# Optimization experiments

Measured on AMD Instinct MI355X. Metric: run time of the kernel, lower is better.

Reference implementation:

```python
import jax, jax.numpy as jnp
import numpy as np

N_ROOMS = 126          # len(building.rooms)
N = 2 + N_ROOMS        # state dim (reset_iv: 2 + n_rooms)
M = 1 + N_ROOMS        # input dim u = [Tout, Q_watts...]
T = 200000             # number of eval times
DT = 30.0              # seconds between eval points
TOUT_DT = 3600.0       # outside-temp table grid spacing (s)
K = 1700               # table length (covers 1000 + T*DT seconds)
LOAD_MAX = 500.0       # physical_loads_scaling: W/m^2 upper bound


def setup_inputs() -> dict:
    key = jax.random.key(0)
    ks = jax.random.split(key, 6)
    # Stable RC-style state matrix: negative diagonal dominates
    A = 1e-5 * jax.random.normal(ks[0], (N, N), dtype=jnp.float32) - 2e-4 * jnp.eye(N, dtype=jnp.float32)
    B = 1e-6 * jax.random.normal(ks[1], (N, M), dtype=jnp.float32)
    loads = jax.random.normal(ks[2], (2, N_ROOMS), dtype=jnp.float32)   # raw params (pre-sigmoid)
    areas = 10.0 + 40.0 * jax.random.uniform(ks[3], (N_ROOMS,), dtype=jnp.float32)  # room areas m^2
    Tout_vals = 10.0 + 5.0 * jax.random.normal(ks[4], (K,), dtype=jnp.float32)      # hourly Tout table
    t_eval = 1000.0 + DT * jnp.arange(T, dtype=jnp.float32)
    iv = 26.0 * jnp.ones((N, 1), dtype=jnp.float32)
    return {"A": A, "B": B, "loads": loads, "areas": areas,
            "Tout_vals": Tout_vals, "t_eval": t_eval, "iv": iv, "action": 1}


def _interp_tout(vals, t):
    # linear interpolation on a uniform grid starting at t=0 (replaces scipy interp1d)
    pos = t / TOUT_DT
    idx = jnp.clip(jnp.floor(pos).astype(jnp.int32), 0, K - 2)
    w = pos - idx.astype(pos.dtype)
    return vals[idx] * (1.0 - w) + vals[idx + 1] * w


def reference(A, B, loads, areas, Tout_vals, t_eval, iv, action):
    t0 = t_eval[0]
    ts = t_eval - t0
    # _build_loads: sigmoid transform + physical scaling
    lp = jax.nn.sigmoid(loads) * LOAD_MAX
    cool_load, gain_load = lp[0], lp[1]
    # f_ode constants: Q_area = -cool*action + gain; Q_watts = proportional_heating
    Q_watts = (-cool_load * action + gain_load) * areas        # [n_rooms]
    b_q = B[:, 1:] @ Q_watts                                   # [N] constant forcing
    b_T = B[:, 0]                                              # [N] Tout coupling
    x0 = iv[:, 0]

    def f(t, x):
        Tout = _interp_tout(Tout_vals, t + t0)
        return A @ x + b_T * Tout + b_q

    # torchdiffeq method='rk4' -> rk4_alt_step_func (3/8 rule)
    def step(x, tt):
        t, tn = tt
        dt = tn - t
        k1 = f(t, x)
        k2 = f(t + dt / 3.0, x + dt * k1 / 3.0)
        k3 = f(t + dt * 2.0 / 3.0, x + dt * (k2 - k1 / 3.0))
        k4 = f(t + dt, x + dt * (k1 - k2 + k3))
        xn = x + dt * (k1 + 3.0 * (k2 + k3) + k4) / 8.0
        return xn, xn

    _, traj = jax.lax.scan(step, x0, (ts[:-1], ts[1:]))
    out = jnp.concatenate([x0[None, :], traj], axis=0)         # [T, N]
    return out[..., None]                                      # [T, N, 1] matching iv shape
```

## Files before the change

### kernel.cpp

```cpp
#include <hip/hip_runtime.h>

#define N 128
#define NR 126
#define MBCOL 127
#define TSTEPS 200000
#define L1 49
#define C1 4096
#define KT 1700

#define OFF_Z     0
#define OFF_S     16384
#define OFF_P     32768
#define OFF_PW2   65536
#define OFF_PW4   81920
#define OFF_PW8   98304
#define OFF_PW16  114688
#define OFF_PW32  131072
#define OFF_Q     147456
#define OFF_WC    180224
#define OFF_ACC   212992
#define OFF_DELTA 737280
#define OFF_B1    753664
#define OFF_B2    1015808
#define OFF_B3    1146880
#define OFF_A16   1212416
#define OFF_C1    1245184
#define OFF_C2    1261568
#define OFF_C3    1269760
#define OFF_BST16 753664
#define OFF_Q256  786432

typedef float v4f __attribute__((ext_vector_type(4)));
typedef __attribute__((ext_vector_type(8))) short bf16x8;
typedef __attribute__((ext_vector_type(4))) float f32x4;

#define OFF_PEH   65536
#define OFF_PEL   75776

#define LBAR() do { \
  __builtin_amdgcn_sched_barrier(0); \
  asm volatile("s_waitcnt lgkmcnt(0)" ::: "memory"); \
  __builtin_amdgcn_sched_barrier(0); \
  __builtin_amdgcn_s_barrier(); \
  __builtin_amdgcn_sched_barrier(0); \
} while (0)

#define GLD4(dst, p) \
  asm volatile("global_load_dwordx4 %0, %1, off" : "=v"(dst) : "v"(p))
#define PINQ(q) \
  asm volatile("s_waitcnt vmcnt(0)" \
    : "+v"(q[0]),"+v"(q[1]),"+v"(q[2]),"+v"(q[3]), \
      "+v"(q[4]),"+v"(q[5]),"+v"(q[6]),"+v"(q[7]), \
      "+v"(q[8]),"+v"(q[9]),"+v"(q[10]),"+v"(q[11]), \
      "+v"(q[12]),"+v"(q[13]),"+v"(q[14]),"+v"(q[15]))
#define PINQ8(q) \
  asm volatile("s_waitcnt vmcnt(0)" \
    : "+v"(q[0]),"+v"(q[1]),"+v"(q[2]),"+v"(q[3]), \
      "+v"(q[4]),"+v"(q[5]),"+v"(q[6]),"+v"(q[7]))

__device__ __forceinline__ void loadQ16(v4f* qv, const float* pb)
{
  #pragma unroll
  for (int s = 0; s < 16; ++s) GLD4(qv[s], pb + 4*s);
  PINQ(qv);
}

__device__ __forceinline__ void bsplit(float f, unsigned short& h, unsigned short& l)
{
  unsigned int u = __float_as_uint(f);
  unsigned int r = (u + 0x7FFFu + ((u >> 16) & 1u)) >> 16;
  float hf = __uint_as_float(r << 16);
  h = (unsigned short)r;
  float lo = f - hf;
  unsigned int u2 = __float_as_uint(lo);
  unsigned int r2 = (u2 + 0x7FFFu + ((u2 >> 16) & 1u)) >> 16;
  l = (unsigned short)r2;
}

__device__ __forceinline__ void mmRowS(const float* __restrict__ Aw,
                                       const float* __restrict__ Bw,
                                       float* __restrict__ Cw,
                                       float* __restrict__ Cw2,
                                       float* __restrict__ sm, int r, float scale)
{
  int t = threadIdx.x, c = t & 127, kh = t >> 7;
  const float* Ar = Aw + r*N + kh*64;
  const float* Bc = Bw + (kh*64)*N + c;
  float p0=0.f, p1=0.f, p2=0.f, p3=0.f;
  #pragma unroll 4
  for (int s = 0; s < 64; s += 4) {
    const float4 av = *(const float4*)(Ar + s);
    p0 = fmaf(av.x, Bc[(s+0)*N], p0);
    p1 = fmaf(av.y, Bc[(s+1)*N], p1);
    p2 = fmaf(av.z, Bc[(s+2)*N], p2);
    p3 = fmaf(av.w, Bc[(s+3)*N], p3);
  }
  sm[kh*128 + c] = (p0+p1)+(p2+p3);
  __syncthreads();
  if (kh == 0) {
    float v = (sm[c] + sm[128 + c]) * scale;
    Cw[r*N + c] = v;
    if (Cw2) Cw2[r*N + c] = v;
  }
}

#define mmRowR(Aw,Bw,Cw,Cw2,sm,r) mmRowS(Aw,Bw,Cw,Cw2,sm,r,1.0f)

__device__ void prepLite(const float* __restrict__ A, const float* __restrict__ B,
                         const float* __restrict__ loads, const float* __restrict__ areas,
                         const float* __restrict__ iv, const int* __restrict__ action,
                         float* __restrict__ ws, float* __restrict__ out,
                         float* __restrict__ sm)
{
  float* qw = sm;
  float* ys = sm + 128;
  float* qs = sm + 640;
  int t = threadIdx.x;
  float actf = (float)action[0];
  if (t < NR) {
    float lc = (1.0f / (1.0f + expf(-loads[t]))) * 500.0f;
    float lg = (1.0f / (1.0f + expf(-loads[NR + t]))) * 500.0f;
    qw[t] = (-lc * actf + lg) * areas[t];
  }
  __syncthreads();
  if (t < N) {
    float bq = 0.0f;
    for (int i = 0; i < NR; ++i) bq += B[t * MBCOL + 1 + i] * qw[i];
    ys[t] = B[t * MBCOL];
    qs[t] = bq;
  }
  __syncthreads();
  for (int s = 1; s < 4; ++s) {
    if (t < N) {
      float ay = 0.0f, aq = 0.0f;
      for (int k = 0; k < N; ++k) {
        float a = A[t * N + k];
        ay += a * ys[(s-1)*N + k];
        aq += a * qs[(s-1)*N + k];
      }
      ys[s*N + t] = 30.0f * ay;
      qs[s*N + t] = 30.0f * aq;
    }
    __syncthreads();
  }
  if (t < N) {
    float y0 = ys[t], y1 = ys[N+t], y2 = ys[2*N+t], y3 = ys[3*N+t];
    float q0 = qs[t], q1 = qs[N+t], q2 = qs[2*N+t], q3 = qs[3*N+t];
    ws[OFF_WC + (0*L1)*N + t] = 3.75f * (y0 + y1 + y2*(1.0f/3.0f) + y3*(1.0f/3.0f));
    ws[OFF_WC + (1*L1)*N + t] = 3.75f * (3.0f*y0 + 2.0f*y1 + y2);
    ws[OFF_WC + (2*L1)*N + t] = 3.75f * (3.0f*y0 + y1);
    ws[OFF_WC + (3*L1)*N + t] = 3.75f * y0;
    ws[OFF_WC + (4*L1)*N + t] = 3.75f * (8.0f*q0 + 4.0f*q1 + (4.0f/3.0f)*q2 + (1.0f/3.0f)*q3);
    out[t] = iv[t];
  }
}

__device__ __forceinline__ void polyRowA(const float* __restrict__ A,
                                         float* __restrict__ ws,
                                         float* __restrict__ sm)
{
  int t = threadIdx.x, c = t & 127, kh = t >> 7;
  int r = blockIdx.x;
  const float* S = ws + OFF_S;
  const float* Sr = S + r*N + kh*64;
  float x3=0.f, x4=0.f;
  #pragma unroll 4
  for (int s = 0; s < 64; s += 4) {
    const float4 av = *(const float4*)(Sr + s);
    int k = kh*64 + s;
    x3 = fmaf(av.x, A[(k+0)*N+c], x3); x3 = fmaf(av.y, A[(k+1)*N+c], x3);
    x3 = fmaf(av.z, A[(k+2)*N+c], x3); x3 = fmaf(av.w, A[(k+3)*N+c], x3);
    x4 = fmaf(av.x, S[(k+0)*N+c], x4); x4 = fmaf(av.y, S[(k+1)*N+c], x4);
    x4 = fmaf(av.z, S[(k+2)*N+c], x4); x4 = fmaf(av.w, S[(k+3)*N+c], x4);
  }
  sm[kh*128 + c] = x3;
  sm[256 + kh*128 + c] = x4;
  __syncthreads();
  if (kh == 0) {
    float a3 = 30.0f * (sm[c] + sm[128+c]);
    float a4 = sm[256+c] + sm[384+c];
    float pv = (r==c ? 1.0f : 0.0f) + 30.0f*A[r*N+c] + 0.5f*S[r*N+c]
             + (1.0f/6.0f)*a3 + (1.0f/24.0f)*a4;
    ws[OFF_P + r*N + c] = pv;
  }
}

__device__ __forceinline__ void wUnit(const float* __restrict__ Pw,
                                      float* __restrict__ ws,
                                      int uw, int wbase, int wcount,
                                      float* __restrict__ wbuf )
{
  int t = threadIdx.x;
  int np = 5 * wcount;
  for (int i = t; i < 8*N; i += 256) {
    int pl = i >> 7, k = i & 127;
    int p = uw*8 + pl;
    float v = 0.0f;
    if (p < np) {
      int m = p / wcount, kk = p % wcount;
      v = ws[OFF_WC + (m*L1 + kk)*N + k];
    }
    wbuf[pl*N + k] = v;
  }
  __syncthreads();
  int r = t & 127, pg = t >> 7;
  float acc[4] = {0,0,0,0};
  #pragma unroll 2
  for (int k = 0; k < N; k += 4) {
    const float4 av = *(const float4*)(Pw + r*N + k);
    #pragma unroll
    for (int pi = 0; pi < 4; ++pi) {
      const float4 wv = *(const float4*)(wbuf + (pg*4+pi)*N + k);
      acc[pi] = fmaf(av.x, wv.x, acc[pi]);
      acc[pi] = fmaf(av.y, wv.y, acc[pi]);
      acc[pi] = fmaf(av.z, wv.z, acc[pi]);
      acc[pi] = fmaf(av.w, wv.w, acc[pi]);
    }
  }
  #pragma unroll
  for (int pi = 0; pi < 4; ++pi) {
    int p = uw*8 + pg*4 + pi;
    if (p < np) {
      int m = p / wcount, kk = p % wcount;
      ws[OFF_WC + (m*L1 + wbase + kk)*N + r] = acc[pi];
    }
  }
}

__device__ __forceinline__ void treeUnit(const float* __restrict__ Qm,
                                         const float* __restrict__ src,
                                         float* __restrict__ dst,
                                         int uw, float* __restrict__ wbuf)
{
  int t = threadIdx.x;
  for (int i = t; i < 8*N; i += 256) {
    int pl = i >> 7, k = i & 127;
    wbuf[pl*N + k] = src[(size_t)(2*(uw*8 + pl))*N + k];
  }
  __syncthreads();
  int r = t & 127, pg = t >> 7;
  float acc[4] = {0,0,0,0};
  #pragma unroll 2
  for (int k = 0; k < N; k += 4) {
    const float4 av = *(const float4*)(Qm + r*N + k);
    #pragma unroll
    for (int pi = 0; pi < 4; ++pi) {
      const float4 wv = *(const float4*)(wbuf + (pg*4+pi)*N + k);
      acc[pi] = fmaf(av.x, wv.x, acc[pi]);
      acc[pi] = fmaf(av.y, wv.y, acc[pi]);
      acc[pi] = fmaf(av.z, wv.z, acc[pi]);
      acc[pi] = fmaf(av.w, wv.w, acc[pi]);
    }
  }
  #pragma unroll
  for (int pi = 0; pi < 4; ++pi) {
    int j = uw*8 + pg*4 + pi;
    dst[(size_t)j*N + r] = acc[pi] + src[(size_t)(2*j + 1)*N + r];
  }
}

__global__ __launch_bounds__(256) void kPhase(
    const float* __restrict__ A, const float* __restrict__ B,
    const float* __restrict__ loads, const float* __restrict__ areas,
    const float* __restrict__ iv, const int* __restrict__ action,
    float* __restrict__ ws, float* __restrict__ out, int ph)
{
  __shared__ float sm[1280];
  int b = blockIdx.x;
  if (ph >= 20) {
    int lv = ph - 20;
    const int srcO[7] = {OFF_ACC, OFF_B1, OFF_B2, OFF_B3, OFF_A16, OFF_C1, OFF_C2};
    const int dstO[7] = {OFF_B1, OFF_B2, OFF_B3, OFF_A16, OFF_C1, OFF_C2, OFF_C3};
    const int nco[7]  = {2048, 1024, 512, 256, 128, 64, 32};
    const int qO[7]   = {OFF_Q, OFF_S, OFF_P, OFF_PW8, OFF_PW16, OFF_PW32, OFF_Z};
    const int pS[7]   = {OFF_S, OFF_P, OFF_PW8, OFF_PW16, OFF_PW32, OFF_Z, OFF_DELTA};
    const int pD[7]   = {OFF_P, OFF_PW8, OFF_PW16, OFF_PW32, OFF_Z, OFF_DELTA, OFF_Q256};
    int nb = nco[lv] >> 3;
    if (b < nb) treeUnit(ws + qO[lv], ws + srcO[lv], ws + dstO[lv], b, sm);
    else mmRowR(ws + pS[lv], ws + pS[lv], ws + pD[lv], nullptr, sm, b - nb);
    return;
  }
  if (ph == 1) {
    if (b < 128) mmRowS(A, A, ws+OFF_S, nullptr, sm, b, 900.0f);
    else prepLite(A, B, loads, areas, iv, action, ws, out, sm);
    return;
  }
  if (ph == 2) { polyRowA(A, ws, sm); return; }
  if (ph <= 8) {
    int s = ph - 3;
    const int srcOff[6] = {OFF_P, OFF_PW2, OFF_PW4, OFF_PW8, OFF_PW16, OFF_PW32};
    const int dstOff[6] = {OFF_PW2, OFF_PW4, OFF_PW8, OFF_PW16, OFF_PW32, OFF_S};
    if (b < 128) {
      if (s < 5) mmRowR(ws+srcOff[s], ws+srcOff[s], ws+dstOff[s], nullptr, sm, b);
      else       mmRowR(ws+OFF_PW32, ws+OFF_PW16, ws+OFF_S, nullptr, sm, b);
    } else {
      int wbase  = (s < 5) ? (1 << s) : 32;
      int wcount = (s < 5) ? (1 << s) : 17;
      wUnit(ws + srcOff[s], ws, b - 128, wbase, wcount, sm);
    }
    return;
  }
  if (ph == 9) {
    if (b < 128) {
      mmRowR(ws+OFF_S, ws+OFF_P, ws+OFF_Z, ws+OFF_Q, sm, b);
    } else {
      int r = b - 128;
      int tt = threadIdx.x;
      if (tt < 160) {
        float val;
        if (tt < 128)      val = ws[OFF_P + r*N + tt];
        else if (tt < 133) val = ws[OFF_WC + ((tt-128)*L1)*N + r];
        else               val = 0.0f;
        unsigned short h, l2;
        bsplit(val, h, l2);
        ((unsigned short*)(ws + OFF_PEH))[r*160 + tt] = h;
        ((unsigned short*)(ws + OFF_PEL))[r*160 + tt] = l2;
      }
    }
    return;
  }
}

__device__ __forceinline__ void build_table(float* lt, const float* __restrict__ Tout,
                                            int J0, int t, int cnt, int stride)
{
  int tbase = 1470*J0 + 1000;
  for (int s = t; s < cnt; s += stride) {
    float tt = (float)(tbase + 10*s);
    float pos = tt / 3600.0f;
    int idx = (int)pos;
    if (idx > KT-2) idx = KT-2;
    float w = pos - (float)idx;
    lt[s] = Tout[idx]*(1.0f-w) + Tout[idx+1]*w;
  }
}

__global__ __launch_bounds__(256) void k3_acc(const float* __restrict__ Tout,
                                              float* __restrict__ ws)
{
  __shared__ float lt[1184];
  int t = threadIdx.x;
  if (blockIdx.x >= 512) {
    mmRowR(ws+OFF_Z, ws+OFF_Z, ws+OFF_S, nullptr, lt, blockIdx.x - 512);
    return;
  }
  int J0 = blockIdx.x * 8;
  build_table(lt, Tout, J0, t, 1177, 256);
  __syncthreads();
  int r = t & 127, jh = t >> 7;
  float a[4] = {0.0f, 0.0f, 0.0f, 0.0f};
  for (int k = 0; k < L1; ++k) {
    float w0 = ws[OFF_WC + (0*L1+k)*N + r];
    float w1 = ws[OFF_WC + (1*L1+k)*N + r];
    float w2 = ws[OFF_WC + (2*L1+k)*N + r];
    float w3 = ws[OFF_WC + (3*L1+k)*N + r];
    float w4 = ws[OFF_WC + (4*L1+k)*N + r];
    #pragma unroll
    for (int q = 0; q < 4; ++q) {
      int cl = jh*4 + q;
      int soff = 3*(L1*cl + (L1-1) - k);
      a[q] += w0*lt[soff] + w1*lt[soff+1] + w2*lt[soff+2] + w3*lt[soff+3] + w4;
    }
  }
  #pragma unroll
  for (int q = 0; q < 4; ++q)
    ws[OFF_ACC + (size_t)(J0 + jh*4 + q)*N + r] = a[q];
}

__device__ __forceinline__ void mv_step3(const v4f* qv, float* x, float* ps,
                                         int r, int kh, float addv)
{
  const v4f* xp = (const v4f*)(x + kh*64);
  float p0=0.f, p1=0.f, p2=0.f, p3=0.f;
  #pragma unroll
  for (int s = 0; s < 16; s += 4) {
    v4f x0 = xp[s+0], x1 = xp[s+1], x2 = xp[s+2], x3 = xp[s+3];
    p0 = fmaf(qv[s+0][0],x0[0],p0); p0 = fmaf(qv[s+0][1],x0[1],p0);
    p0 = fmaf(qv[s+0][2],x0[2],p0); p0 = fmaf(qv[s+0][3],x0[3],p0);
    p1 = fmaf(qv[s+1][0],x1[0],p1); p1 = fmaf(qv[s+1][1],x1[1],p1);
    p1 = fmaf(qv[s+1][2],x1[2],p1); p1 = fmaf(qv[s+1][3],x1[3],p1);
    p2 = fmaf(qv[s+2][0],x2[0],p2); p2 = fmaf(qv[s+2][1],x2[1],p2);
    p2 = fmaf(qv[s+2][2],x2[2],p2); p2 = fmaf(qv[s+2][3],x2[3],p2);
    p3 = fmaf(qv[s+3][0],x3[0],p3); p3 = fmaf(qv[s+3][1],x3[1],p3);
    p3 = fmaf(qv[s+3][2],x3[2],p3); p3 = fmaf(qv[s+3][3],x3[3],p3);
  }
  ps[kh*128 + r] = (p0+p1)+(p2+p3);
  LBAR();
  if (kh == 0) x[r] = ps[r] + ps[128 + r] + addv;
  LBAR();
}

__global__ __launch_bounds__(256, 2) void k5ab(const float* __restrict__ iv,
                                               float* __restrict__ ws)
{
  __shared__ float x[N];
  __shared__ float ps[256];
  __shared__ float c3[32*N];
  __shared__ float aq[15*N];
  __shared__ float a16d[15*N];
  int t = threadIdx.x, r = t & 127, kh = t >> 7;
  int p = blockIdx.x;
  for (int i = t; i < 32*N; i += 256) c3[i] = ws[OFF_C3 + i];
  for (int i = t; i < 15*N; i += 256) a16d[i] = ws[OFF_A16 + (size_t)(p*16)*N + i];
  if (t < N) x[t] = iv[t];
  v4f qv[16];
  loadQ16(qv, ws + OFF_DELTA + r*N + kh*64);
  __syncthreads();
  for (int q = 0; q < p; ++q) {
    const v4f* xp = (const v4f*)(c3 + (size_t)(2*q)*N + kh*64);
    float p0=0.f, p1=0.f, p2=0.f, p3=0.f;
    #pragma unroll
    for (int s = 0; s < 16; s += 4) {
      v4f x0 = xp[s+0], x1 = xp[s+1], x2 = xp[s+2], x3 = xp[s+3];
      p0 = fmaf(qv[s+0][0],x0[0],p0); p0 = fmaf(qv[s+0][1],x0[1],p0);
      p0 = fmaf(qv[s+0][2],x0[2],p0); p0 = fmaf(qv[s+0][3],x0[3],p0);
      p1 = fmaf(qv[s+1][0],x1[0],p1); p1 = fmaf(qv[s+1][1],x1[1],p1);
      p1 = fmaf(qv[s+1][2],x1[2],p1); p1 = fmaf(qv[s+1][3],x1[3],p1);
      p2 = fmaf(qv[s+2][0],x2[0],p2); p2 = fmaf(qv[s+2][1],x2[1],p2);
      p2 = fmaf(qv[s+2][2],x2[2],p2); p2 = fmaf(qv[s+2][3],x2[3],p2);
      p3 = fmaf(qv[s+3][0],x3[0],p3); p3 = fmaf(qv[s+3][1],x3[1],p3);
      p3 = fmaf(qv[s+3][2],x3[2],p3); p3 = fmaf(qv[s+3][3],x3[3],p3);
    }
    ps[kh*128 + r] = (p0+p1)+(p2+p3);
    LBAR();
    if (kh == 0) aq[q*N + r] = ps[r] + ps[128 + r] + c3[(size_t)(2*q+1)*N + r];
    LBAR();
  }
  loadQ16(qv, ws + OFF_Q256 + r*N + kh*64);
  __syncthreads();
  for (int q = 0; q < p; ++q)
    mv_step3(qv, x, ps, r, kh, aq[q*N + r]);
  loadQ16(qv, ws + OFF_PW16 + r*N + kh*64);
  __syncthreads();
  for (int i = 0; i < 16; ++i) {
    if (kh == 0) ws[OFF_BST16 + (size_t)(p*16 + i)*N + r] = x[r];
    if (i == 15) break;
    mv_step3(qv, x, ps, r, kh, a16d[i*N + r]);
  }
}

__global__ __launch_bounds__(512) void k7_main(const float* __restrict__ Tout,
                                               const float* __restrict__ ws,
                                               float* __restrict__ out)
{
  __shared__ float ltp[3136];
  __shared__ __align__(16) unsigned short XbHi[2][16][168];
  __shared__ __align__(16) unsigned short XbLo[2][16][168];
  __shared__ float xf[N];
  __shared__ float psf[512];
  int t = threadIdx.x;
  int m = blockIdx.x;
  int J0 = m * 16;

  for (int e = t; e < 3136; e += 512) {
    int cl = e / 196, rem = e - cl*196;
    int i = rem >> 2, mm = rem & 3;
    float tt = (float)(1000 + 1470*(J0 + cl) + 30*i + 10*mm);
    float pos = tt / 3600.0f;
    int idx = (int)pos;
    if (idx > KT-2) idx = KT-2;
    float w = pos - (float)idx;
    ltp[e] = Tout[idx]*(1.0f-w) + Tout[idx+1]*w;
  }
  for (int e = t; e < 2*16*40; e += 512) {
    int bu = e / 640, rem = e - bu*640;
    int cn = rem / 40, k = 128 + (rem - cn*40);
    XbHi[bu][cn][k] = 0; XbLo[bu][cn][k] = 0;
  }
  __syncthreads();
  if (t < 80) {
    int cn = t / 5, mm = t - cn*5;
    float v = (mm < 4) ? ltp[cn*196 + mm] : 1.0f;
    unsigned short h, l2; bsplit(v, h, l2);
    XbHi[0][cn][128+mm] = h; XbLo[0][cn][128+mm] = l2;
  }

  int r = t & 127, kq = t >> 7;
  v4f q8[8];
  #pragma unroll
  for (int s = 0; s < 8; ++s) GLD4(q8[s], ws + OFF_Q + r*N + kq*32 + 4*s);
  PINQ8(q8);
  if (t < N) xf[t] = ws[OFF_BST16 + (size_t)m*N + t];
  __syncthreads();
  float nxtA = (t < N) ? ws[OFF_ACC + (size_t)(J0)*N + t] : 0.0f;
  for (int c = 0; c < 16; ++c) {
    if (t < N) {
      unsigned short h, l2; bsplit(xf[t], h, l2);
      XbHi[0][c][t] = h; XbLo[0][c][t] = l2;
    }
    if (c == 15) { LBAR(); break; }
    float pp0 = 0.f, pp1 = 0.f;
    const v4f* xp = (const v4f*)(xf + kq*32);
    #pragma unroll
    for (int s = 0; s < 8; s += 2) {
      v4f x0 = xp[s], x1 = xp[s+1];
      pp0 = fmaf(q8[s][0],x0[0],pp0);   pp0 = fmaf(q8[s][1],x0[1],pp0);
      pp0 = fmaf(q8[s][2],x0[2],pp0);   pp0 = fmaf(q8[s][3],x0[3],pp0);
      pp1 = fmaf(q8[s+1][0],x1[0],pp1); pp1 = fmaf(q8[s+1][1],x1[1],pp1);
      pp1 = fmaf(q8[s+1][2],x1[2],pp1); pp1 = fmaf(q8[s+1][3],x1[3],pp1);
    }
    psf[t] = pp0 + pp1;
    LBAR();
    if (t < N) {
      float addv = nxtA;
      nxtA = ws[OFF_ACC + (size_t)(J0 + c + 1)*N + t];
      xf[t] = psf[t] + psf[t+128] + psf[t+256] + psf[t+384] + addv;
    }
    LBAR();
  }

  int l = t & 63, w = t >> 6;
  int la = l & 15, lg = l >> 4;
  int rowA = w*16 + la;
  const unsigned short* peh = (const unsigned short*)(ws + OFF_PEH);
  const unsigned short* pel = (const unsigned short*)(ws + OFF_PEL);
  bf16x8 Ah[5], Al[5];
  #pragma unroll
  for (int kt = 0; kt < 5; ++kt) {
    Ah[kt] = *(const bf16x8*)(peh + rowA*160 + kt*32 + lg*8);
    Al[kt] = *(const bf16x8*)(pel + rowA*160 + kt*32 + lg*8);
  }

  int rowD = w*16 + lg*4;
  int nnB = L1*(J0 + la);
  for (int i = 0; i < L1; ++i) {
    int cur = i & 1, nxt = cur ^ 1;
    bf16x8 Bh[5], Bl[5];
    #pragma unroll
    for (int kt = 0; kt < 5; ++kt) {
      Bh[kt] = *(const bf16x8*)(&XbHi[cur][la][kt*32 + lg*8]);
      Bl[kt] = *(const bf16x8*)(&XbLo[cur][la][kt*32 + lg*8]);
    }
    f32x4 ahh = {0.f,0.f,0.f,0.f}, ahl = {0.f,0.f,0.f,0.f}, alh = {0.f,0.f,0.f,0.f};
    #pragma unroll
    for (int kt = 0; kt < 5; ++kt) {
      ahh = __builtin_amdgcn_mfma_f32_16x16x32_bf16(Ah[kt], Bh[kt], ahh, 0, 0, 0);
      ahl = __builtin_amdgcn_mfma_f32_16x16x32_bf16(Ah[kt], Bl[kt], ahl, 0, 0, 0);
      alh = __builtin_amdgcn_mfma_f32_16x16x32_bf16(Al[kt], Bh[kt], alh, 0, 0, 0);
    }
    f32x4 y = ahh + ahl + alh;
    int nn = nnB + i + 1;
    if (nn < TSTEPS)
      *(f32x4*)(out + (size_t)nn*N + rowD) = y;
    unsigned short h0,h1,h2,h3,q0,q1,q2,q3;
    bsplit(y[0],h0,q0); bsplit(y[1],h1,q1); bsplit(y[2],h2,q2); bsplit(y[3],h3,q3);
    unsigned int hA = (unsigned)h0 | ((unsigned)h1<<16);
    unsigned int hB = (unsigned)h2 | ((unsigned)h3<<16);
    unsigned int lA = (unsigned)q0 | ((unsigned)q1<<16);
    unsigned int lB = (unsigned)q2 | ((unsigned)q3<<16);
    *reinterpret_cast<uint2*>(&XbHi[nxt][la][rowD]) = make_uint2(hA, hB);
    *reinterpret_cast<uint2*>(&XbLo[nxt][la][rowD]) = make_uint2(lA, lB);
    if (t < 80 && i < L1-1) {
      int cn = t / 5, mm = t - cn*5;
      float v = (mm < 4) ? ltp[cn*196 + (i+1)*4 + mm] : 1.0f;
      unsigned short hh, ll; bsplit(v, hh, ll);
      XbHi[nxt][cn][128+mm] = hh; XbLo[nxt][cn][128+mm] = ll;
    }
    LBAR();
  }
}

extern "C" void kernel_launch(void* const* d_in, const int* in_sizes, int n_in,
                              void* d_out, int out_size, void* d_ws, size_t ws_size,
                              hipStream_t stream)
{
  const float* A     = (const float*)d_in[0];
  const float* B     = (const float*)d_in[1];
  const float* loads = (const float*)d_in[2];
  const float* areas = (const float*)d_in[3];
  const float* Tout  = (const float*)d_in[4];
  const float* iv    = (const float*)d_in[6];
  const int* action  = (const int*)d_in[7];
  float* out = (float*)d_out;
  float* ws  = (float*)d_ws;

  const int phGrid[10] = {0, 129, 128, 129, 130, 131, 133, 138, 139, 256};
  for (int ph = 1; ph <= 9; ++ph)
    hipLaunchKernelGGL(kPhase, dim3(phGrid[ph]), dim3(256), 0, stream,
                       A, B, loads, areas, iv, action, ws, out, ph);
  hipLaunchKernelGGL(k3_acc, dim3(640), dim3(256), 0, stream, Tout, ws);
  const int trGrid[7] = {384, 256, 192, 160, 144, 136, 132};
  for (int lv = 0; lv < 7; ++lv)
    hipLaunchKernelGGL(kPhase, dim3(trGrid[lv]), dim3(256), 0, stream,
                       A, B, loads, areas, iv, action, ws, out, 20 + lv);
  hipLaunchKernelGGL(k5ab,   dim3(16),  dim3(256), 0, stream, iv, ws);
  hipLaunchKernelGGL(k7_main, dim3(256), dim3(512), 0, stream, Tout, ws, out);
}
```

Before: 216.3 us.

## Fuse tree-reduction levels and k5ab into one persistent kernel with atomic barriers

```diff
diff --git a/kernel.cpp b/kernel.cpp
--- a/kernel.cpp
+++ b/kernel.cpp
@@ -29,6 +29,7 @@
 #define OFF_C3    1269760
 #define OFF_BST16 753664
 #define OFF_Q256  786432
+#define OFF_CNT   1277952
 
 typedef float v4f __attribute__((ext_vector_type(4)));
 typedef __attribute__((ext_vector_type(8))) short bf16x8;
@@ -267,44 +268,31 @@
 {
   __shared__ float sm[1280];
   int b = blockIdx.x;
-  if (ph >= 20) {
-    int lv = ph - 20;
-    const int srcO[7] = {OFF_ACC, OFF_B1, OFF_B2, OFF_B3, OFF_A16, OFF_C1, OFF_C2};
-    const int dstO[7] = {OFF_B1, OFF_B2, OFF_B3, OFF_A16, OFF_C1, OFF_C2, OFF_C3};
-    const int nco[7]  = {2048, 1024, 512, 256, 128, 64, 32};
-    const int qO[7]   = {OFF_Q, OFF_S, OFF_P, OFF_PW8, OFF_PW16, OFF_PW32, OFF_Z};
-    const int pS[7]   = {OFF_S, OFF_P, OFF_PW8, OFF_PW16, OFF_PW32, OFF_Z, OFF_DELTA};
-    const int pD[7]   = {OFF_P, OFF_PW8, OFF_PW16, OFF_PW32, OFF_Z, OFF_DELTA, OFF_Q256};
-    int nb = nco[lv] >> 3;
-    if (b < nb) treeUnit(ws + qO[lv], ws + srcO[lv], ws + dstO[lv], b, sm);
-    else mmRowR(ws + pS[lv], ws + pS[lv], ws + pD[lv], nullptr, sm, b - nb);
-    return;
-  }
   if (ph == 1) {
     if (b < 128) mmRowS(A, A, ws+OFF_S, nullptr, sm, b, 900.0f);
     else prepLite(A, B, loads, areas, iv, action, ws, out, sm);
     return;
   }
   if (ph == 2) { polyRowA(A, ws, sm); return; }
-  if (ph <= 8) {
+  if (ph <= 6) {
     int s = ph - 3;
-    const int srcOff[6] = {OFF_P, OFF_PW2, OFF_PW4, OFF_PW8, OFF_PW16, OFF_PW32};
-    const int dstOff[6] = {OFF_PW2, OFF_PW4, OFF_PW8, OFF_PW16, OFF_PW32, OFF_S};
-    if (b < 128) {
-      if (s < 5) mmRowR(ws+srcOff[s], ws+srcOff[s], ws+dstOff[s], nullptr, sm, b);
-      else       mmRowR(ws+OFF_PW32, ws+OFF_PW16, ws+OFF_S, nullptr, sm, b);
-    } else {
-      int wbase  = (s < 5) ? (1 << s) : 32;
-      int wcount = (s < 5) ? (1 << s) : 17;
-      wUnit(ws + srcOff[s], ws, b - 128, wbase, wcount, sm);
-    }
+    const int srcOff[4] = {OFF_P, OFF_PW2, OFF_PW4, OFF_PW8};
+    const int dstOff[4] = {OFF_PW2, OFF_PW4, OFF_PW8, OFF_PW16};
+    if (b < 128) mmRowR(ws+srcOff[s], ws+srcOff[s], ws+dstOff[s], nullptr, sm, b);
+    else wUnit(ws + srcOff[s], ws, b - 128, 1 << s, 1 << s, sm);
     return;
   }
-  if (ph == 9) {
-    if (b < 128) {
-      mmRowR(ws+OFF_S, ws+OFF_P, ws+OFF_Z, ws+OFF_Q, sm, b);
-    } else {
-      int r = b - 128;
+  if (ph == 7) {
+    if (b < 128)      mmRowR(ws+OFF_PW16, ws+OFF_PW16, ws+OFF_PW32, nullptr, sm, b);
+    else if (b < 256) mmRowR(ws+OFF_PW16, ws+OFF_P, ws+OFF_DELTA, nullptr, sm, b - 128);
+    else              wUnit(ws+OFF_PW16, ws, b - 256, 16, 16, sm);
+    return;
+  }
+  {
+    if (b < 128)      mmRowR(ws+OFF_PW32, ws+OFF_DELTA, ws+OFF_Z, ws+OFF_Q, sm, b);
+    else if (b < 139) wUnit(ws+OFF_PW32, ws, b - 128, 32, 17, sm);
+    else {
+      int r = b - 139;
       int tt = threadIdx.x;
       if (tt < 160) {
         float val;
@@ -317,7 +305,6 @@
         ((unsigned short*)(ws + OFF_PEL))[r*160 + tt] = l2;
       }
     }
-    return;
   }
 }
 
@@ -340,6 +327,8 @@
 {
   __shared__ float lt[1184];
   int t = threadIdx.x;
+  if (blockIdx.x == 0 && t < 8)
+    ((int*)(ws + OFF_CNT))[t] = 0;
   if (blockIdx.x >= 512) {
     mmRowR(ws+OFF_Z, ws+OFF_Z, ws+OFF_S, nullptr, lt, blockIdx.x - 512);
     return;
@@ -390,16 +379,15 @@
   LBAR();
 }
 
-__global__ __launch_bounds__(256, 2) void k5ab(const float* __restrict__ iv,
-                                               float* __restrict__ ws)
-{
-  __shared__ float x[N];
-  __shared__ float ps[256];
-  __shared__ float c3[32*N];
-  __shared__ float aq[15*N];
-  __shared__ float a16d[15*N];
+__device__ void k5Tail(const float* __restrict__ iv, float* __restrict__ ws,
+                       float* __restrict__ sm, int p)
+{
+  float* x    = sm;
+  float* ps   = sm + 128;
+  float* c3   = sm + 384;
+  float* aq   = sm + 4480;
+  float* a16d = sm + 6400;
   int t = threadIdx.x, r = t & 127, kh = t >> 7;
-  int p = blockIdx.x;
   for (int i = t; i < 32*N; i += 256) c3[i] = ws[OFF_C3 + i];
   for (int i = t; i < 15*N; i += 256) a16d[i] = ws[OFF_A16 + (size_t)(p*16)*N + i];
   if (t < N) x[t] = iv[t];
@@ -437,6 +425,48 @@
     if (i == 15) break;
     mv_step3(qv, x, ps, r, kh, a16d[i*N + r]);
   }
+}
+
+__global__ __launch_bounds__(256, 2) void kTree(const float* __restrict__ iv,
+                                                float* __restrict__ ws)
+{
+  __shared__ float sm[8448];
+  int b = blockIdx.x, t = threadIdx.x;
+  int* cnt = (int*)(ws + OFF_CNT);
+  const int srcO[7] = {OFF_ACC, OFF_B1, OFF_B2, OFF_B3, OFF_A16, OFF_C1, OFF_C2};
+  const int dstO[7] = {OFF_B1, OFF_B2, OFF_B3, OFF_A16, OFF_C1, OFF_C2, OFF_C3};
+  const int nbA[7]  = {256, 128, 64, 32, 16, 8, 4};
+  const int qO[7]   = {OFF_Q, OFF_S, OFF_P, OFF_PW8, OFF_PW16, OFF_PW32, OFF_Z};
+  const int pS[7]   = {OFF_S, OFF_P, OFF_PW8, OFF_PW16, OFF_PW32, OFF_Z, OFF_DELTA};
+  const int pD[7]   = {OFF_P, OFF_PW8, OFF_PW16, OFF_PW32, OFF_Z, OFF_DELTA, OFF_Q256};
+  for (int lv = 0; lv < 7; ++lv) {
+    if (lv > 0) {
+      int need = nbA[lv-1] + 128;
+      if (t == 0) {
+        while (__hip_atomic_load(&cnt[lv-1], __ATOMIC_ACQUIRE,
+                                 __HIP_MEMORY_SCOPE_AGENT) < need)
+          __builtin_amdgcn_s_sleep(1);
+      }
+      __syncthreads();
+    }
+    int nb = nbA[lv];
+    if (b < nb)
+      treeUnit(ws + qO[lv], ws + srcO[lv], ws + dstO[lv], b, sm);
+    else if (b < nb + 128)
+      mmRowR(ws + pS[lv], ws + pS[lv], ws + pD[lv], nullptr, sm, b - nb);
+    __syncthreads();
+    if (b < nb + 128 && t == 0)
+      __hip_atomic_fetch_add(&cnt[lv], 1, __ATOMIC_RELEASE,
+                             __HIP_MEMORY_SCOPE_AGENT);
+  }
+  if (b >= 16) return;
+  if (t == 0) {
+    while (__hip_atomic_load(&cnt[6], __ATOMIC_ACQUIRE,
+                             __HIP_MEMORY_SCOPE_AGENT) < 132)
+      __builtin_amdgcn_s_sleep(1);
+  }
+  __syncthreads();
+  k5Tail(iv, ws, sm, b);
 }
 
 __global__ __launch_bounds__(512) void k7_main(const float* __restrict__ Tout,
@@ -574,15 +604,11 @@
   float* out = (float*)d_out;
   float* ws  = (float*)d_ws;
 
-  const int phGrid[10] = {0, 129, 128, 129, 130, 131, 133, 138, 139, 256};
-  for (int ph = 1; ph <= 9; ++ph)
+  const int phGrid[9] = {0, 129, 128, 129, 130, 131, 133, 266, 267};
+  for (int ph = 1; ph <= 8; ++ph)
     hipLaunchKernelGGL(kPhase, dim3(phGrid[ph]), dim3(256), 0, stream,
                        A, B, loads, areas, iv, action, ws, out, ph);
   hipLaunchKernelGGL(k3_acc, dim3(640), dim3(256), 0, stream, Tout, ws);
-  const int trGrid[7] = {384, 256, 192, 160, 144, 136, 132};
-  for (int lv = 0; lv < 7; ++lv)
-    hipLaunchKernelGGL(kPhase, dim3(trGrid[lv]), dim3(256), 0, stream,
-                       A, B, loads, areas, iv, action, ws, out, 20 + lv);
-  hipLaunchKernelGGL(k5ab,   dim3(16),  dim3(256), 0, stream, iv, ws);
+  hipLaunchKernelGGL(kTree,  dim3(384), dim3(256), 0, stream, iv, ws);
   hipLaunchKernelGGL(k7_main, dim3(256), dim3(512), 0, stream, Tout, ws, out);
 }
```

Measured after the change: 570.6 us. +163.8%, slower.
